# Performance work log

Measured on AMD Instinct MI355X. Metric: run time of the kernel, lower is better.

The kernel has to match this reference:

```python
import jax, jax.numpy as jnp
import numpy as np

B = 1024      # batch of samples accumulated
F_DIM = 768   # backbone feature dim (ViT out_dim)
M = 512       # buffer_size (random projection width)
C = 100       # number of classes


def setup_inputs() -> dict:
    key = jax.random.key(0)
    k1, k2, k3 = jax.random.split(key, 3)
    X = jax.random.normal(k1, (B, F_DIM), dtype=jnp.float32)
    # RandomBuffer weight (fixed random projection), Linear-style init scale
    W = jax.random.normal(k2, (F_DIM, M), dtype=jnp.float32) / np.float32(np.sqrt(F_DIM))
    labels = jax.random.randint(k3, (B,), 0, C)  # argmax(Y, dim=1)
    return {"X": X, "W": W, "labels": labels}


def reference(X, W, labels):
    # RandomBuffer.forward: relu(X @ W) -> [B, M]
    feat = jax.nn.relu(X @ W)
    # per-sample outer product f^T f, scatter-added per class label
    outer = feat[:, :, None] * feat[:, None, :]          # [B, M, M]
    phi = jax.ops.segment_sum(outer, labels, num_segments=C)   # [C, M, M]
    mu = jax.ops.segment_sum(feat, labels, num_segments=C)     # [C, M]
    count = jax.ops.segment_sum(jnp.ones((B,), feat.dtype), labels, num_segments=C)  # [C]
    return phi, mu, count
```

## Files before the change

kernel.cpp:

```cpp
#include <hip/hip_runtime.h>

#define B_N    1024
#define F_DIMC 768
#define M_DIM  512
#define C_N    100
#define KSTEP  32
#define NSTEP  (F_DIMC / KSTEP)
#define NGEMM  512
#define NIDX   25

typedef float f32x4 __attribute__((ext_vector_type(4)));
typedef short s16x8 __attribute__((ext_vector_type(8)));

__device__ __forceinline__ unsigned int cvt_pk_bf16(float lo, float hi) {
  unsigned int r;
  asm("v_cvt_pk_bf16_f32 %0, %1, %2" : "=v"(r) : "v"(lo), "v"(hi));
  return r;
}

__global__ __launch_bounds__(256) void gemm_index_kernel(
    const float* __restrict__ X, const float* __restrict__ W,
    const int* __restrict__ labels, float* __restrict__ feat,
    int* __restrict__ counts, int* __restrict__ idx) {
  __shared__ unsigned short Ah[2][32][40], Al[2][32][40];
  __shared__ unsigned short Bh[2][32][40], Bl[2][32][40];
  __shared__ int lab[B_N];

  const int t = threadIdx.x;
  const int b = (int)blockIdx.x;

  if (b >= NGEMM) {
    for (int i = t; i < B_N; i += 256) lab[i] = labels[i];
    __syncthreads();
    const int w    = t >> 6;
    const int lane = t & 63;
    const int c    = (b - NGEMM) * 4 + w;
    if (c < C_N) {
      int base = 0;
      for (int ch = 0; ch < 16; ++ch) {
        const int j = ch * 64 + lane;
        const bool hit = (lab[j] == c);
        const unsigned long long mask = __ballot(hit);
        if (hit) {
          const int r = __popcll(mask & ((1ull << lane) - 1ull));
          idx[c * B_N + base + r] = j;
        }
        base += __popcll(mask);
      }
      if (lane == 0) counts[c] = base;
    }
    return;
  }

  const int bm = (b >> 4) * 32;
  const int bn = (b & 15) * 32;

  const bool isX = (t < 128);
  const int xr = t >> 2;
  const int xk = (t & 3) * 8;
  const int uu = isX ? 0 : (t - 128);
  const int wk = (uu >> 3) * 2;
  const int wc = (uu & 7) * 4;

  const float* __restrict__ Xp = X + (size_t)(bm + xr) * F_DIMC + xk;
  const float* __restrict__ Wp = W + (size_t)wk * M_DIM + bn + wc;

  const int lane = t & 63;
  const int wv   = t >> 6;
  const int m0 = (wv & 1) * 16;
  const int n0 = (wv >> 1) * 16;
  const int fr = lane & 15;
  const int fq = (lane >> 4) * 8;

  f32x4 acc = {0.f, 0.f, 0.f, 0.f};

  float4 ra0, ra1, rb0, rb1;
  if (isX) {
    ra0 = *(const float4*)(Xp);
    ra1 = *(const float4*)(Xp + 4);
  } else {
    rb0 = *(const float4*)(Wp);
    rb1 = *(const float4*)(Wp + M_DIM);
  }

  auto STAGE = [&](int buf) {
    if (isX) {
      const float v[8] = {ra0.x, ra0.y, ra0.z, ra0.w,
                          ra1.x, ra1.y, ra1.z, ra1.w};
      unsigned int hu[4], lu[4];
#pragma unroll
      for (int j = 0; j < 4; ++j) {
        hu[j] = cvt_pk_bf16(v[2 * j], v[2 * j + 1]);
        const float l0 =
            v[2 * j] - __builtin_bit_cast(float, hu[j] << 16);
        const float l1 =
            v[2 * j + 1] - __builtin_bit_cast(float, hu[j] & 0xffff0000u);
        lu[j] = cvt_pk_bf16(l0, l1);
      }
      *(uint4*)&Ah[buf][xr][xk] = make_uint4(hu[0], hu[1], hu[2], hu[3]);
      *(uint4*)&Al[buf][xr][xk] = make_uint4(lu[0], lu[1], lu[2], lu[3]);
    } else {
      const float a[4] = {rb0.x, rb0.y, rb0.z, rb0.w};
      const float d[4] = {rb1.x, rb1.y, rb1.z, rb1.w};
#pragma unroll
      for (int i = 0; i < 4; ++i) {
        const unsigned int h = cvt_pk_bf16(a[i], d[i]);
        const float la = a[i] - __builtin_bit_cast(float, h << 16);
        const float ld = d[i] - __builtin_bit_cast(float, h & 0xffff0000u);
        const unsigned int l = cvt_pk_bf16(la, ld);
        *(unsigned int*)&Bh[buf][wc + i][wk] = h;
        *(unsigned int*)&Bl[buf][wc + i][wk] = l;
      }
    }
  };

  STAGE(0);
  __syncthreads();

  for (int it = 0; it < NSTEP; ++it) {
    const int cur = it & 1;
    if (it + 1 < NSTEP) {
      const int k0 = (it + 1) * KSTEP;
      if (isX) {
        ra0 = *(const float4*)(Xp + k0);
        ra1 = *(const float4*)(Xp + k0 + 4);
      } else {
        rb0 = *(const float4*)(Wp + (size_t)k0 * M_DIM);
        rb1 = *(const float4*)(Wp + (size_t)(k0 + 1) * M_DIM);
      }
    }
    const s16x8 ah = *(const s16x8*)&Ah[cur][m0 + fr][fq];
    const s16x8 al = *(const s16x8*)&Al[cur][m0 + fr][fq];
    const s16x8 bh = *(const s16x8*)&Bh[cur][n0 + fr][fq];
    const s16x8 bl = *(const s16x8*)&Bl[cur][n0 + fr][fq];
    acc = __builtin_amdgcn_mfma_f32_16x16x32_bf16(ah, bh, acc, 0, 0, 0);
    acc = __builtin_amdgcn_mfma_f32_16x16x32_bf16(al, bh, acc, 0, 0, 0);
    acc = __builtin_amdgcn_mfma_f32_16x16x32_bf16(ah, bl, acc, 0, 0, 0);
    if (it + 1 < NSTEP) STAGE(cur ^ 1);
    __syncthreads();
  }

  const int r0 = (lane >> 4) * 4;
#pragma unroll
  for (int r = 0; r < 4; ++r)
    feat[(size_t)(bm + m0 + r0 + r) * M_DIM + bn + n0 + fr] =
        fmaxf(acc[r], 0.0f);
}

__global__ __launch_bounds__(256, 4) void phi_mu_kernel(
    const float* __restrict__ feat, const int* __restrict__ counts,
    const int* __restrict__ idx, float* __restrict__ phi,
    float* __restrict__ mu, float* __restrict__ cnt_out) {
  const int c = blockIdx.y;
  const int n = counts[c];
  const int* __restrict__ id = idx + c * B_N;
  const int t = threadIdx.x;

  if (blockIdx.x == 16) {
    float2 acc = make_float2(0.f, 0.f);
    for (int s = 0; s < n; ++s) {
      const float2 q = *(const float2*)&feat[(size_t)id[s] * M_DIM + t * 2];
      acc.x += q.x;
      acc.y += q.y;
    }
    *(float2*)&mu[(size_t)c * M_DIM + t * 2] = acc;
    if (t == 0) cnt_out[c] = (float)n;
    return;
  }

  const int px = (int)blockIdx.x;
  const int tr = t >> 6;
  const int tc = t & 63;

  __shared__ float F[16][M_DIM];

  float acc[8][8] = {};

  for (int s0 = 0; s0 < n; s0 += 16) {
    const int chunk  = min(16, n - s0);
    if (s0) __syncthreads();
    const int nslots = chunk << 7;
    for (int v = t; v < nslots; v += 256) {
      const int sl = v >> 7;
      const int fp = (v & 127) << 2;
      *(float4*)&F[sl][fp] =
          *(const float4*)&feat[(size_t)id[s0 + sl] * M_DIM + fp];
    }
    __syncthreads();
    for (int sl = 0; sl < chunk; ++sl) {
      const float4 a0 = *(const float4*)&F[sl][px * 32 + tr * 8];
      const float4 a1 = *(const float4*)&F[sl][px * 32 + tr * 8 + 4];
      const float4 b0 = *(const float4*)&F[sl][tc * 4];
      const float4 b1 = *(const float4*)&F[sl][256 + tc * 4];
      const float av[8] = {a0.x, a0.y, a0.z, a0.w, a1.x, a1.y, a1.z, a1.w};
      const float bv[8] = {b0.x, b0.y, b0.z, b0.w, b1.x, b1.y, b1.z, b1.w};
#pragma unroll
      for (int r = 0; r < 8; ++r)
#pragma unroll
        for (int q = 0; q < 8; ++q)
          acc[r][q] += av[r] * bv[q];
    }
  }

  float* __restrict__ out = phi + (size_t)c * M_DIM * M_DIM;
#pragma unroll
  for (int r = 0; r < 8; ++r) {
    const size_t row = (size_t)(px * 32 + tr * 8 + r) * M_DIM;
    const f32x4 o0 = {acc[r][0], acc[r][1], acc[r][2], acc[r][3]};
    const f32x4 o1 = {acc[r][4], acc[r][5], acc[r][6], acc[r][7]};
    __builtin_nontemporal_store(o0, (f32x4*)&out[row + tc * 4]);
    __builtin_nontemporal_store(o1, (f32x4*)&out[row + 256 + tc * 4]);
  }
}

extern "C" void kernel_launch(void* const* d_in, const int* in_sizes, int n_in,
                              void* d_out, int out_size, void* d_ws,
                              size_t ws_size, hipStream_t stream) {
  const float* X      = (const float*)d_in[0];
  const float* W      = (const float*)d_in[1];
  const int*   labels = (const int*)d_in[2];

  float* out = (float*)d_out;
  float* phi = out;
  float* mu  = out + (size_t)C_N * M_DIM * M_DIM;
  float* cnt = mu + (size_t)C_N * M_DIM;

  float* feat   = (float*)d_ws;
  int*   counts = (int*)((char*)d_ws + (size_t)B_N * M_DIM * sizeof(float));
  int*   idx    = counts + 128;

  hipLaunchKernelGGL(gemm_index_kernel, dim3(NGEMM + NIDX), dim3(256), 0,
                     stream, X, W, labels, feat, counts, idx);
  hipLaunchKernelGGL(phi_mu_kernel, dim3(17, C_N), dim3(256), 0, stream,
                     feat, counts, idx, phi, mu, cnt);
}
```

Before: 41.41 us.

## Split GEMM K dimension in two with larger 64x64 tiles, fuse ReLU into consumer

The feature GEMM now uses 512-thread blocks with 64x64 output tiles, and each block covers half of the K dimension (split-K by 2), giving 256 GEMM blocks. Each block writes raw partial sums to a workspace. The phi/mu kernel adds the two partials and applies ReLU when it loads feature rows. The aim is to shorten the serial K loop per block and get more reuse per tile. The cost is twice the workspace traffic and double global reads in the consumer kernel.

Result: faster. 39.34 us (-5.0%).

```diff
diff --git a/kernel.cpp b/kernel.cpp
--- a/kernel.cpp
+++ b/kernel.cpp
@@ -4,10 +4,11 @@
 #define F_DIMC 768
 #define M_DIM  512
 #define C_N    100
+#define KHALF  (F_DIMC / 2)
 #define KSTEP  32
-#define NSTEP  (F_DIMC / KSTEP)
-#define NGEMM  512
-#define NIDX   25
+#define NSTEP2 (KHALF / KSTEP)
+#define NGEMM  256
+#define NIDX   13
 
 typedef float f32x4 __attribute__((ext_vector_type(4)));
 typedef short s16x8 __attribute__((ext_vector_type(8)));
@@ -17,24 +18,30 @@
   asm("v_cvt_pk_bf16_f32 %0, %1, %2" : "=v"(r) : "v"(lo), "v"(hi));
   return r;
 }
-
-__global__ __launch_bounds__(256) void gemm_index_kernel(
+__device__ __forceinline__ float bflo(unsigned int u) {
+  return __builtin_bit_cast(float, u << 16);
+}
+__device__ __forceinline__ float bfhi(unsigned int u) {
+  return __builtin_bit_cast(float, u & 0xffff0000u);
+}
+
+__global__ __launch_bounds__(512) void gemm_index_kernel(
     const float* __restrict__ X, const float* __restrict__ W,
-    const int* __restrict__ labels, float* __restrict__ feat,
+    const int* __restrict__ labels, float* __restrict__ part,
     int* __restrict__ counts, int* __restrict__ idx) {
-  __shared__ unsigned short Ah[2][32][40], Al[2][32][40];
-  __shared__ unsigned short Bh[2][32][40], Bl[2][32][40];
+  __shared__ unsigned short Ah[2][64][40], Al[2][64][40];
+  __shared__ unsigned short Bh[2][64][40], Bl[2][64][40];
   __shared__ int lab[B_N];
 
   const int t = threadIdx.x;
   const int b = (int)blockIdx.x;
 
   if (b >= NGEMM) {
-    for (int i = t; i < B_N; i += 256) lab[i] = labels[i];
+    for (int i = t; i < B_N; i += 512) lab[i] = labels[i];
     __syncthreads();
     const int w    = t >> 6;
     const int lane = t & 63;
-    const int c    = (b - NGEMM) * 4 + w;
+    const int c    = (b - NGEMM) * 8 + w;
     if (c < C_N) {
       int base = 0;
       for (int ch = 0; ch < 16; ++ch) {
@@ -52,27 +59,32 @@
     return;
   }
 
-  const int bm = (b >> 4) * 32;
-  const int bn = (b & 15) * 32;
-
-  const bool isX = (t < 128);
+  const int kb   = b >> 7;
+  const int tile = b & 127;
+  const int bm = (tile >> 3) * 64;
+  const int bn = (tile & 7) * 64;
+
+  const bool isX = (t < 256);
   const int xr = t >> 2;
   const int xk = (t & 3) * 8;
-  const int uu = isX ? 0 : (t - 128);
-  const int wk = (uu >> 3) * 2;
-  const int wc = (uu & 7) * 4;
-
-  const float* __restrict__ Xp = X + (size_t)(bm + xr) * F_DIMC + xk;
-  const float* __restrict__ Wp = W + (size_t)wk * M_DIM + bn + wc;
+  const int uu = isX ? 0 : (t - 256);
+  const int wk = (uu >> 4) * 2;
+  const int wc = (uu & 15) * 4;
+
+  const float* __restrict__ Xp =
+      X + (size_t)(bm + xr) * F_DIMC + kb * KHALF + xk;
+  const float* __restrict__ Wp =
+      W + (size_t)(kb * KHALF + wk) * M_DIM + bn + wc;
 
   const int lane = t & 63;
   const int wv   = t >> 6;
-  const int m0 = (wv & 1) * 16;
-  const int n0 = (wv >> 1) * 16;
+  const int m0 = (wv & 3) * 16;
+  const int nh = wv >> 2;
   const int fr = lane & 15;
   const int fq = (lane >> 4) * 8;
 
-  f32x4 acc = {0.f, 0.f, 0.f, 0.f};
+  f32x4 acc0 = {0.f, 0.f, 0.f, 0.f};
+  f32x4 acc1 = {0.f, 0.f, 0.f, 0.f};
 
   float4 ra0, ra1, rb0, rb1;
   if (isX) {
@@ -91,10 +103,8 @@
 #pragma unroll
       for (int j = 0; j < 4; ++j) {
         hu[j] = cvt_pk_bf16(v[2 * j], v[2 * j + 1]);
-        const float l0 =
-            v[2 * j] - __builtin_bit_cast(float, hu[j] << 16);
-        const float l1 =
-            v[2 * j + 1] - __builtin_bit_cast(float, hu[j] & 0xffff0000u);
+        const float l0 = v[2 * j] - bflo(hu[j]);
+        const float l1 = v[2 * j + 1] - bfhi(hu[j]);
         lu[j] = cvt_pk_bf16(l0, l1);
       }
       *(uint4*)&Ah[buf][xr][xk] = make_uint4(hu[0], hu[1], hu[2], hu[3]);
@@ -105,8 +115,8 @@
 #pragma unroll
       for (int i = 0; i < 4; ++i) {
         const unsigned int h = cvt_pk_bf16(a[i], d[i]);
-        const float la = a[i] - __builtin_bit_cast(float, h << 16);
-        const float ld = d[i] - __builtin_bit_cast(float, h & 0xffff0000u);
+        const float la = a[i] - bflo(h);
+        const float ld = d[i] - bfhi(h);
         const unsigned int l = cvt_pk_bf16(la, ld);
         *(unsigned int*)&Bh[buf][wc + i][wk] = h;
         *(unsigned int*)&Bl[buf][wc + i][wk] = l;
@@ -117,9 +127,9 @@
   STAGE(0);
   __syncthreads();
 
-  for (int it = 0; it < NSTEP; ++it) {
+  for (int it = 0; it < NSTEP2; ++it) {
     const int cur = it & 1;
-    if (it + 1 < NSTEP) {
+    if (it + 1 < NSTEP2) {
       const int k0 = (it + 1) * KSTEP;
       if (isX) {
         ra0 = *(const float4*)(Xp + k0);
@@ -131,26 +141,39 @@
     }
     const s16x8 ah = *(const s16x8*)&Ah[cur][m0 + fr][fq];
     const s16x8 al = *(const s16x8*)&Al[cur][m0 + fr][fq];
-    const s16x8 bh = *(const s16x8*)&Bh[cur][n0 + fr][fq];
-    const s16x8 bl = *(const s16x8*)&Bl[cur][n0 + fr][fq];
-    acc = __builtin_amdgcn_mfma_f32_16x16x32_bf16(ah, bh, acc, 0, 0, 0);
-    acc = __builtin_amdgcn_mfma_f32_16x16x32_bf16(al, bh, acc, 0, 0, 0);
-    acc = __builtin_amdgcn_mfma_f32_16x16x32_bf16(ah, bl, acc, 0, 0, 0);
-    if (it + 1 < NSTEP) STAGE(cur ^ 1);
+    {
+      const s16x8 bh = *(const s16x8*)&Bh[cur][(nh * 2) * 16 + fr][fq];
+      const s16x8 bl = *(const s16x8*)&Bl[cur][(nh * 2) * 16 + fr][fq];
+      acc0 = __builtin_amdgcn_mfma_f32_16x16x32_bf16(ah, bh, acc0, 0, 0, 0);
+      acc0 = __builtin_amdgcn_mfma_f32_16x16x32_bf16(al, bh, acc0, 0, 0, 0);
+      acc0 = __builtin_amdgcn_mfma_f32_16x16x32_bf16(ah, bl, acc0, 0, 0, 0);
+    }
+    {
+      const s16x8 bh = *(const s16x8*)&Bh[cur][(nh * 2 + 1) * 16 + fr][fq];
+      const s16x8 bl = *(const s16x8*)&Bl[cur][(nh * 2 + 1) * 16 + fr][fq];
+      acc1 = __builtin_amdgcn_mfma_f32_16x16x32_bf16(ah, bh, acc1, 0, 0, 0);
+      acc1 = __builtin_amdgcn_mfma_f32_16x16x32_bf16(al, bh, acc1, 0, 0, 0);
+      acc1 = __builtin_amdgcn_mfma_f32_16x16x32_bf16(ah, bl, acc1, 0, 0, 0);
+    }
+    if (it + 1 < NSTEP2) STAGE(cur ^ 1);
     __syncthreads();
   }
 
-  const int r0 = (lane >> 4) * 4;
-#pragma unroll
-  for (int r = 0; r < 4; ++r)
-    feat[(size_t)(bm + m0 + r0 + r) * M_DIM + bn + n0 + fr] =
-        fmaxf(acc[r], 0.0f);
+  float* __restrict__ dst = part + (size_t)kb * B_N * M_DIM;
+  const int rr0 = (lane >> 4) * 4;
+#pragma unroll
+  for (int r = 0; r < 4; ++r) {
+    const size_t row = (size_t)(bm + m0 + rr0 + r) * M_DIM;
+    dst[row + bn + (nh * 2) * 16 + fr]     = acc0[r];
+    dst[row + bn + (nh * 2 + 1) * 16 + fr] = acc1[r];
+  }
 }
 
 __global__ __launch_bounds__(256, 4) void phi_mu_kernel(
-    const float* __restrict__ feat, const int* __restrict__ counts,
-    const int* __restrict__ idx, float* __restrict__ phi,
-    float* __restrict__ mu, float* __restrict__ cnt_out) {
+    const float* __restrict__ p0, const float* __restrict__ p1,
+    const int* __restrict__ counts, const int* __restrict__ idx,
+    float* __restrict__ phi, float* __restrict__ mu,
+    float* __restrict__ cnt_out) {
   const int c = blockIdx.y;
   const int n = counts[c];
   const int* __restrict__ id = idx + c * B_N;
@@ -159,9 +182,11 @@
   if (blockIdx.x == 16) {
     float2 acc = make_float2(0.f, 0.f);
     for (int s = 0; s < n; ++s) {
-      const float2 q = *(const float2*)&feat[(size_t)id[s] * M_DIM + t * 2];
-      acc.x += q.x;
-      acc.y += q.y;
+      const size_t o = (size_t)id[s] * M_DIM + t * 2;
+      const float2 q0 = *(const float2*)&p0[o];
+      const float2 q1 = *(const float2*)&p1[o];
+      acc.x += fmaxf(q0.x + q1.x, 0.f);
+      acc.y += fmaxf(q0.y + q1.y, 0.f);
     }
     *(float2*)&mu[(size_t)c * M_DIM + t * 2] = acc;
     if (t == 0) cnt_out[c] = (float)n;
@@ -181,10 +206,17 @@
     if (s0) __syncthreads();
     const int nslots = chunk << 7;
     for (int v = t; v < nslots; v += 256) {
-      const int sl = v >> 7;
-      const int fp = (v & 127) << 2;
-      *(float4*)&F[sl][fp] =
-          *(const float4*)&feat[(size_t)id[s0 + sl] * M_DIM + fp];
+      const int sl   = v >> 7;
+      const int fp   = (v & 127) << 2;
+      const size_t o = (size_t)id[s0 + sl] * M_DIM + fp;
+      const float4 q0 = *(const float4*)&p0[o];
+      const float4 q1 = *(const float4*)&p1[o];
+      float4 f;
+      f.x = fmaxf(q0.x + q1.x, 0.f);
+      f.y = fmaxf(q0.y + q1.y, 0.f);
+      f.z = fmaxf(q0.z + q1.z, 0.f);
+      f.w = fmaxf(q0.w + q1.w, 0.f);
+      *(float4*)&F[sl][fp] = f;
     }
     __syncthreads();
     for (int sl = 0; sl < chunk; ++sl) {
@@ -225,12 +257,13 @@
   float* mu  = out + (size_t)C_N * M_DIM * M_DIM;
   float* cnt = mu + (size_t)C_N * M_DIM;
 
-  float* feat   = (float*)d_ws;
-  int*   counts = (int*)((char*)d_ws + (size_t)B_N * M_DIM * sizeof(float));
+  float* part   = (float*)d_ws;
+  int*   counts = (int*)((char*)d_ws + (size_t)2 * B_N * M_DIM * sizeof(float));
   int*   idx    = counts + 128;
 
-  hipLaunchKernelGGL(gemm_index_kernel, dim3(NGEMM + NIDX), dim3(256), 0,
-                     stream, X, W, labels, feat, counts, idx);
+  hipLaunchKernelGGL(gemm_index_kernel, dim3(NGEMM + NIDX), dim3(512), 0,
+                     stream, X, W, labels, part, counts, idx);
   hipLaunchKernelGGL(phi_mu_kernel, dim3(17, C_N), dim3(256), 0, stream,
-                     feat, counts, idx, phi, mu, cnt);
-}
+                     part, part + (size_t)B_N * M_DIM, counts, idx,
+                     phi, mu, cnt);
+}
```
